# Performance work log

Measured on AMD Instinct MI355X. Metric: run time of the kernel, lower is better.

## Reference

```python
import jax, jax.numpy as jnp
import numpy as np

B, S, IN_DIM, EMBED, H = 2, 2048, 512, 512, 8
HD = EMBED // H


def setup_inputs() -> dict:
    key = jax.random.key(0)
    ks = jax.random.split(key, 6)
    x = jax.random.normal(ks[0], (B, S, IN_DIM), dtype=jnp.float32)
    dist_mat = jax.random.normal(ks[1], (B, H, S, S), dtype=jnp.float32) * 0.02
    path_mat = jax.random.normal(ks[2], (B, H, S, S), dtype=jnp.float32) * 0.02
    # xavier-uniform-style init scale
    qkv_w = jax.random.normal(ks[3], (IN_DIM, 3 * EMBED), dtype=jnp.float32) * (1.0 / np.sqrt(IN_DIM))
    qkv_b = jnp.zeros((3 * EMBED,), dtype=jnp.float32)
    o_w = jax.random.normal(ks[4], (EMBED, EMBED), dtype=jnp.float32) * (1.0 / np.sqrt(EMBED))
    o_b = jnp.zeros((EMBED,), dtype=jnp.float32)
    return {"x": x, "dist_mat": dist_mat, "path_mat": path_mat,
            "qkv_w": qkv_w, "qkv_b": qkv_b, "o_w": o_w, "o_b": o_b}


def reference(x, dist_mat, path_mat, qkv_w, qkv_b, o_w, o_b):
    b, s, _ = x.shape
    qkv = x @ qkv_w + qkv_b                         # [B,S,3*EMBED]
    qkv = qkv.reshape(b, s, H, 3 * HD).transpose(0, 2, 1, 3)  # [B,H,S,3*HD]
    q, k, v = jnp.split(qkv, 3, axis=-1)            # each [B,H,S,HD]
    logits = jnp.einsum('bhqd,bhkd->bhqk', q, k) / jnp.sqrt(jnp.float32(HD))
    attn = jax.nn.softmax(logits, axis=-1)
    attn = attn + dist_mat + path_mat               # post-softmax bias (breaks flash fusion)
    vals = jnp.einsum('bhqk,bhkd->bhqd', attn, v)   # [B,H,S,HD]
    vals = vals.transpose(0, 2, 1, 3).reshape(b, s, EMBED)
    return vals @ o_w + o_b
```

## Files before the change

kernel.cpp:

```cpp
#include <hip/hip_runtime.h>
#include <stdint.h>
#include <stddef.h>

#define B_ 2
#define H_ 8
#define S_ 2048
#define D_ 64
#define E_ 512
#define N3_ 1536
#define M_ (B_*S_)
#define K_ 512

typedef __attribute__((ext_vector_type(4))) float f32x4;
typedef __attribute__((ext_vector_type(8))) __bf16 bf16x8;
typedef __attribute__((ext_vector_type(4))) __bf16 bf16x4;

static __device__ __forceinline__ int swz(int b) { return b ^ (((b >> 7) & 7) << 4); }

static __device__ __forceinline__ void gl_lds16(const void* g, void* l) {
    __builtin_amdgcn_global_load_lds((const __attribute__((address_space(1))) void*)g,
                                     (__attribute__((address_space(3))) void*)l, 16, 0, 0);
}

__global__ void cvt_bf16_kernel(const float* __restrict__ in, __bf16* __restrict__ out, int n4) {
    int i = blockIdx.x * blockDim.x + threadIdx.x;
    if (i < n4) {
        float4 v = reinterpret_cast<const float4*>(in)[i];
        bf16x4 o;
        o[0] = (__bf16)v.x; o[1] = (__bf16)v.y; o[2] = (__bf16)v.z; o[3] = (__bf16)v.w;
        reinterpret_cast<bf16x4*>(out)[i] = o;
    }
}

__global__ void transpose_cvt_kernel(const float* __restrict__ in, __bf16* __restrict__ out,
                                     int R, int C) {
    __shared__ float tile[32][33];
    int tc = blockIdx.x * 32, tr = blockIdx.y * 32;
    int lx = threadIdx.x & 31, ly = threadIdx.x >> 5;
    #pragma unroll
    for (int p = 0; p < 4; ++p) {
        int r = tr + ly + p * 8, c = tc + lx;
        if (r < R && c < C) tile[ly + p * 8][lx] = in[(size_t)r * C + c];
    }
    __syncthreads();
    #pragma unroll
    for (int p = 0; p < 4; ++p) {
        int oc = tc + ly + p * 8;
        int orow = tr + lx;
        if (oc < C && orow < R) out[(size_t)oc * R + orow] = (__bf16)tile[lx][ly + p * 8];
    }
}

__global__ void transpose_v_kernel(const __bf16* __restrict__ v, __bf16* __restrict__ vt) {
    __shared__ __bf16 t[64][65];
    int bh = blockIdx.x >> 5;
    int s0 = (blockIdx.x & 31) << 6;
    int tid = threadIdx.x;
    const __bf16* src = v + ((size_t)bh * S_ + s0) * D_;
    #pragma unroll
    for (int p = 0; p < 2; ++p) {
        int idx = (p * 256 + tid) * 8;
        int r = idx >> 6, c = idx & 63;
        bf16x8 val = *reinterpret_cast<const bf16x8*>(src + (size_t)r * D_ + c);
        #pragma unroll
        for (int e = 0; e < 8; ++e) t[r][c + e] = val[e];
    }
    __syncthreads();
    __bf16* dst = vt + (size_t)bh * D_ * S_ + s0;
    #pragma unroll
    for (int p = 0; p < 16; ++p) {
        int idx = p * 256 + tid;
        int d = idx >> 6, s = idx & 63;
        dst[(size_t)d * S_ + s] = t[s][d];
    }
}

template<int MODE>
__global__ __launch_bounds__(256, 2) void gemm_kernel(
    const __bf16* __restrict__ A, const __bf16* __restrict__ Bt,
    const float* __restrict__ bias,
    void* __restrict__ o0, void* __restrict__ o1, void* __restrict__ o2,
    int M, int N, int K)
{
    __shared__ __align__(16) __bf16 lA[128 * 64];
    __shared__ __align__(16) __bf16 lB[128 * 64];
    const int tid = threadIdx.x;
    const int wave = tid >> 6, lane = tid & 63;
    const int wm = wave >> 1, wn = wave & 1;
    const int m0 = blockIdx.y * 128, n0 = blockIdx.x * 128;
    const int l15 = lane & 15, l4 = lane >> 4;

    f32x4 acc[4][4] = {};

    for (int k0 = 0; k0 < K; k0 += 64) {
        __syncthreads();
        #pragma unroll
        for (int p = 0; p < 4; ++p) {
            int base = p * 4096 + wave * 1024;
            int js = swz(base + lane * 16);
            int row = js >> 7, colb = js & 127;
            gl_lds16((const char*)A + ((size_t)(m0 + row) * K + k0) * 2 + colb, (char*)lA + base);
            gl_lds16((const char*)Bt + ((size_t)(n0 + row) * K + k0) * 2 + colb, (char*)lB + base);
        }
        __syncthreads();
        #pragma unroll
        for (int ks = 0; ks < 2; ++ks) {
            bf16x8 af[4], bfr[4];
            #pragma unroll
            for (int i = 0; i < 4; ++i) {
                af[i]  = *(const bf16x8*)((const char*)lA + swz(((wm * 64 + i * 16 + l15) << 7) + ks * 64 + (l4 << 4)));
                bfr[i] = *(const bf16x8*)((const char*)lB + swz(((wn * 64 + i * 16 + l15) << 7) + ks * 64 + (l4 << 4)));
            }
            #pragma unroll
            for (int i = 0; i < 4; ++i)
                #pragma unroll
                for (int j = 0; j < 4; ++j)
                    acc[i][j] = __builtin_amdgcn_mfma_f32_16x16x32_bf16(af[i], bfr[j], acc[i][j], 0, 0, 0);
        }
    }
    #pragma unroll
    for (int i = 0; i < 4; ++i) {
        int mg0 = m0 + wm * 64 + i * 16 + (l4 << 2);
        #pragma unroll
        for (int j = 0; j < 4; ++j) {
            int ng = n0 + wn * 64 + j * 16 + l15;
            float bv = bias[ng];
            #pragma unroll
            for (int r = 0; r < 4; ++r) {
                int m = mg0 + r;
                float val = acc[i][j][r] + bv;
                if (MODE == 0) {
                    int h = ng / 192, rr = ng % 192;
                    int which = rr >> 6, d = rr & 63;
                    int b = m >> 11, s = m & (S_ - 1);
                    if (which == 0) val *= 0.125f;
                    __bf16* dst = which == 0 ? (__bf16*)o0 : which == 1 ? (__bf16*)o1 : (__bf16*)o2;
                    dst[(((size_t)((b * H_ + h) * S_ + s)) << 6) + d] = (__bf16)val;
                } else {
                    ((float*)o0)[(size_t)m * N + ng] = val;
                }
            }
        }
    }
}

__global__ __launch_bounds__(256, 2) void attn_kernel(
    const __bf16* __restrict__ q, const __bf16* __restrict__ k,
    const __bf16* __restrict__ vt,
    const float* __restrict__ dist, const float* __restrict__ path,
    __bf16* __restrict__ vals)
{
    __shared__ __align__(16) __bf16 kl[64 * 64];
    __shared__ __align__(16) __bf16 vl[64 * 64];
    __shared__ __align__(16) __bf16 pl[4][16 * 64];
    const int tid = threadIdx.x, wave = tid >> 6, lane = tid & 63;
    const int l15 = lane & 15, l4 = lane >> 4;
    const int bh = blockIdx.x >> 5;
    const int q0 = (blockIdx.x & 31) << 6;
    const int b = bh >> 3, h = bh & 7;
    const int qrow = q0 + wave * 16 + l15;

    const __bf16* qp = q + ((size_t)bh * S_ + qrow) * D_;
    bf16x8 qf0 = *(const bf16x8*)(qp + (l4 << 3));
    bf16x8 qf1 = *(const bf16x8*)(qp + 32 + (l4 << 3));

    const float* dp = dist + ((size_t)bh * S_ + qrow) * S_;
    const float* pp = path + ((size_t)bh * S_ + qrow) * S_;

    float m_run[4], l_run[4];
    f32x4 o_p[4] = {}, o_b[4] = {};
    #pragma unroll
    for (int r = 0; r < 4; ++r) { m_run[r] = -1e30f; l_run[r] = 0.f; }

    const char* kg = (const char*)(k + (size_t)bh * S_ * D_);
    const char* vg = (const char*)(vt + (size_t)bh * D_ * S_);

    for (int kt = 0; kt < S_; kt += 64) {
        __syncthreads();
        #pragma unroll
        for (int p = 0; p < 2; ++p) {
            int base = p * 4096 + wave * 1024;
            int js = swz(base + lane * 16);
            int row = js >> 7, colb = js & 127;
            gl_lds16(kg + ((size_t)(kt + row) * D_) * 2 + colb, (char*)kl + base);
            gl_lds16(vg + ((size_t)row * S_ + kt) * 2 + colb, (char*)vl + base);
        }
        float4 dv[2][2], pw[2][2];
        #pragma unroll
        for (int ks = 0; ks < 2; ++ks) {
            int kc = kt + ks * 32 + (l4 << 3);
            dv[ks][0] = *(const float4*)(dp + kc);
            dv[ks][1] = *(const float4*)(dp + kc + 4);
            pw[ks][0] = *(const float4*)(pp + kc);
            pw[ks][1] = *(const float4*)(pp + kc + 4);
        }
        __syncthreads();

        f32x4 lg[4] = {};
        #pragma unroll
        for (int ks = 0; ks < 2; ++ks) {
            bf16x8 qa = ks ? qf1 : qf0;
            #pragma unroll
            for (int n = 0; n < 4; ++n) {
                bf16x8 kf = *(const bf16x8*)((const char*)kl + swz(((n * 16 + l15) << 7) + ks * 64 + (l4 << 4)));
                lg[n] = __builtin_amdgcn_mfma_f32_16x16x32_bf16(qa, kf, lg[n], 0, 0, 0);
            }
        }
        float scale[4], rsum[4], pe[4][4];
        #pragma unroll
        for (int r = 0; r < 4; ++r) {
            float t = fmaxf(fmaxf(lg[0][r], lg[1][r]), fmaxf(lg[2][r], lg[3][r]));
            t = fmaxf(t, __shfl_xor(t, 1));
            t = fmaxf(t, __shfl_xor(t, 2));
            t = fmaxf(t, __shfl_xor(t, 4));
            t = fmaxf(t, __shfl_xor(t, 8));
            float mnew = fmaxf(m_run[r], t);
            scale[r] = __expf(m_run[r] - mnew);
            m_run[r] = mnew;
            rsum[r] = 0.f;
        }
        #pragma unroll
        for (int n = 0; n < 4; ++n)
            #pragma unroll
            for (int r = 0; r < 4; ++r) {
                pe[n][r] = __expf(lg[n][r] - m_run[r]);
                rsum[r] += pe[n][r];
            }
        #pragma unroll
        for (int r = 0; r < 4; ++r) {
            float s = rsum[r];
            s += __shfl_xor(s, 1);
            s += __shfl_xor(s, 2);
            s += __shfl_xor(s, 4);
            s += __shfl_xor(s, 8);
            l_run[r] = l_run[r] * scale[r] + s;
        }
        #pragma unroll
        for (int n = 0; n < 4; ++n)
            #pragma unroll
            for (int r = 0; r < 4; ++r)
                o_p[n][r] *= scale[r];
        char* pb = (char*)&pl[wave][0];
        #pragma unroll
        for (int n = 0; n < 4; ++n)
            #pragma unroll
            for (int r = 0; r < 4; ++r) {
                int row = (l4 << 2) + r, col = n * 16 + l15;
                *(__bf16*)(pb + swz((row << 7) + col * 2)) = (__bf16)pe[n][r];
            }
        #pragma unroll
        for (int ks = 0; ks < 2; ++ks) {
            bf16x8 pa = *(const bf16x8*)((const char*)pb + swz((l15 << 7) + ks * 64 + (l4 << 4)));
            float4 a0 = dv[ks][0], a1 = dv[ks][1], b0 = pw[ks][0], b1 = pw[ks][1];
            bf16x8 ba;
            ba[0] = (__bf16)(a0.x + b0.x); ba[1] = (__bf16)(a0.y + b0.y);
            ba[2] = (__bf16)(a0.z + b0.z); ba[3] = (__bf16)(a0.w + b0.w);
            ba[4] = (__bf16)(a1.x + b1.x); ba[5] = (__bf16)(a1.y + b1.y);
            ba[6] = (__bf16)(a1.z + b1.z); ba[7] = (__bf16)(a1.w + b1.w);
            #pragma unroll
            for (int n = 0; n < 4; ++n) {
                bf16x8 vf = *(const bf16x8*)((const char*)vl + swz(((n * 16 + l15) << 7) + ks * 64 + (l4 << 4)));
                o_p[n] = __builtin_amdgcn_mfma_f32_16x16x32_bf16(pa, vf, o_p[n], 0, 0, 0);
                o_b[n] = __builtin_amdgcn_mfma_f32_16x16x32_bf16(ba, vf, o_b[n], 0, 0, 0);
            }
        }
    }
    #pragma unroll
    for (int r = 0; r < 4; ++r) {
        int s = q0 + wave * 16 + (l4 << 2) + r;
        float inv = 1.f / l_run[r];
        __bf16* dst = vals + (size_t)(b * S_ + s) * E_ + h * D_;
        #pragma unroll
        for (int n = 0; n < 4; ++n) {
            int d = n * 16 + l15;
            dst[d] = (__bf16)(o_p[n][r] * inv + o_b[n][r]);
        }
    }
}

extern "C" void kernel_launch(void* const* d_in, const int* in_sizes, int n_in,
                              void* d_out, int out_size, void* d_ws, size_t ws_size,
                              hipStream_t stream) {
    (void)in_sizes; (void)n_in; (void)out_size; (void)ws_size;
    const float* x      = (const float*)d_in[0];
    const float* dist   = (const float*)d_in[1];
    const float* path   = (const float*)d_in[2];
    const float* qkv_w  = (const float*)d_in[3];
    const float* qkv_b  = (const float*)d_in[4];
    const float* o_w    = (const float*)d_in[5];
    const float* o_b    = (const float*)d_in[6];
    float* out = (float*)d_out;

    char* ws = (char*)d_ws;
    __bf16* xb     = (__bf16*)(ws);
    __bf16* qkv_wT = (__bf16*)(ws + (4  << 20));
    __bf16* o_wT   = (__bf16*)(ws + (6  << 20));
    __bf16* qb     = (__bf16*)(ws + (7  << 20));
    __bf16* kb     = (__bf16*)(ws + (11 << 20));
    __bf16* vb     = (__bf16*)(ws + (15 << 20));
    __bf16* vtb    = (__bf16*)(ws + (19 << 20));
    __bf16* valsb  = (__bf16*)(ws + (23 << 20));

    cvt_bf16_kernel<<<(M_ * K_ / 4 + 255) / 256, 256, 0, stream>>>(x, xb, M_ * K_ / 4);
    transpose_cvt_kernel<<<dim3(N3_ / 32, K_ / 32), 256, 0, stream>>>(qkv_w, qkv_wT, K_, N3_);
    transpose_cvt_kernel<<<dim3(E_ / 32, E_ / 32), 256, 0, stream>>>(o_w, o_wT, E_, E_);
    gemm_kernel<0><<<dim3(N3_ / 128, M_ / 128), 256, 0, stream>>>(xb, qkv_wT, qkv_b, qb, kb, vb, M_, N3_, K_);
    transpose_v_kernel<<<B_ * H_ * (S_ / 64), 256, 0, stream>>>(vb, vtb);
    attn_kernel<<<B_ * H_ * (S_ / 64), 256, 0, stream>>>(qb, kb, vtb, dist, path, valsb);
    gemm_kernel<1><<<dim3(E_ / 128, M_ / 128), 256, 0, stream>>>(valsb, o_wT, o_b, out, nullptr, nullptr, M_, E_, K_);
}
```

Before: 202.3 us.

## Split bias-times-V into separate blocks in a fused launch, combine afterward

Moves the (dist+path)@V product out of the softmax attention loop into its own set of 512 blocks, launched in the same grid as the attention blocks. Bias blocks stream dist/path from global memory and read V^T directly from global. Attention blocks now only do compute-bound QK/softmax/PV. Both write fp32 partial results, and a new combine kernel adds them into bf16 vals. Block IDs are remapped so that each head's work lands on one XCD, and occupancy is raised to 4 blocks per SM. The cost is extra fp32 intermediate traffic and one additional kernel launch.

```diff
diff --git a/kernel.cpp b/kernel.cpp
--- a/kernel.cpp
+++ b/kernel.cpp
@@ -144,31 +144,64 @@
     }
 }
 
-__global__ __launch_bounds__(256, 2) void attn_kernel(
+#define NBIAS 512
+__global__ __launch_bounds__(256, 4) void fused_kernel(
     const __bf16* __restrict__ q, const __bf16* __restrict__ k,
     const __bf16* __restrict__ vt,
     const float* __restrict__ dist, const float* __restrict__ path,
-    __bf16* __restrict__ vals)
+    float* __restrict__ attno, float* __restrict__ biaso)
 {
     __shared__ __align__(16) __bf16 kl[64 * 64];
     __shared__ __align__(16) __bf16 vl[64 * 64];
     __shared__ __align__(16) __bf16 pl[4][16 * 64];
     const int tid = threadIdx.x, wave = tid >> 6, lane = tid & 63;
     const int l15 = lane & 15, l4 = lane >> 4;
-    const int bh = blockIdx.x >> 5;
-    const int q0 = (blockIdx.x & 31) << 6;
-    const int b = bh >> 3, h = bh & 7;
+    const int id = blockIdx.x;
+
+    if (id < NBIAS) {
+        const int xcd = id & 7, j = id >> 3;
+        const int bh = xcd * 2 + (j >> 5), m0 = (j & 31) << 6;
+        const int row = m0 + wave * 16 + l15;
+        const float* dp = dist + ((size_t)bh * S_ + row) * S_;
+        const float* pp = path + ((size_t)bh * S_ + row) * S_;
+        const __bf16* vtp = vt + (size_t)bh * D_ * S_;
+        f32x4 acc[4] = {};
+        #pragma unroll 2
+        for (int k0 = 0; k0 < S_; k0 += 32) {
+            int kc = k0 + (l4 << 3);
+            float4 d0 = *(const float4*)(dp + kc), d1 = *(const float4*)(dp + kc + 4);
+            float4 p0 = *(const float4*)(pp + kc), p1 = *(const float4*)(pp + kc + 4);
+            bf16x8 a;
+            a[0] = (__bf16)(d0.x + p0.x); a[1] = (__bf16)(d0.y + p0.y);
+            a[2] = (__bf16)(d0.z + p0.z); a[3] = (__bf16)(d0.w + p0.w);
+            a[4] = (__bf16)(d1.x + p1.x); a[5] = (__bf16)(d1.y + p1.y);
+            a[6] = (__bf16)(d1.z + p1.z); a[7] = (__bf16)(d1.w + p1.w);
+            #pragma unroll
+            for (int n = 0; n < 4; ++n) {
+                bf16x8 vf = *(const bf16x8*)(vtp + (size_t)(n * 16 + l15) * S_ + kc);
+                acc[n] = __builtin_amdgcn_mfma_f32_16x16x32_bf16(a, vf, acc[n], 0, 0, 0);
+            }
+        }
+        #pragma unroll
+        for (int n = 0; n < 4; ++n)
+            #pragma unroll
+            for (int r = 0; r < 4; ++r)
+                biaso[((size_t)bh * S_ + m0 + wave * 16 + (l4 << 2) + r) * D_ + n * 16 + l15] = acc[n][r];
+        return;
+    }
+
+    const int aid = id - NBIAS;
+    const int xcd = aid & 7, j = aid >> 3;
+    const int bh = xcd * 2 + (j >> 5);
+    const int q0 = (j & 31) << 6;
     const int qrow = q0 + wave * 16 + l15;
 
     const __bf16* qp = q + ((size_t)bh * S_ + qrow) * D_;
     bf16x8 qf0 = *(const bf16x8*)(qp + (l4 << 3));
     bf16x8 qf1 = *(const bf16x8*)(qp + 32 + (l4 << 3));
 
-    const float* dp = dist + ((size_t)bh * S_ + qrow) * S_;
-    const float* pp = path + ((size_t)bh * S_ + qrow) * S_;
-
     float m_run[4], l_run[4];
-    f32x4 o_p[4] = {}, o_b[4] = {};
+    f32x4 o_p[4] = {};
     #pragma unroll
     for (int r = 0; r < 4; ++r) { m_run[r] = -1e30f; l_run[r] = 0.f; }
 
@@ -184,15 +217,6 @@
             int row = js >> 7, colb = js & 127;
             gl_lds16(kg + ((size_t)(kt + row) * D_) * 2 + colb, (char*)kl + base);
             gl_lds16(vg + ((size_t)row * S_ + kt) * 2 + colb, (char*)vl + base);
-        }
-        float4 dv[2][2], pw[2][2];
-        #pragma unroll
-        for (int ks = 0; ks < 2; ++ks) {
-            int kc = kt + ks * 32 + (l4 << 3);
-            dv[ks][0] = *(const float4*)(dp + kc);
-            dv[ks][1] = *(const float4*)(dp + kc + 4);
-            pw[ks][0] = *(const float4*)(pp + kc);
-            pw[ks][1] = *(const float4*)(pp + kc + 4);
         }
         __syncthreads();
 
@@ -245,23 +269,16 @@
         for (int n = 0; n < 4; ++n)
             #pragma unroll
             for (int r = 0; r < 4; ++r) {
-                int row = (l4 << 2) + r, col = n * 16 + l15;
-                *(__bf16*)(pb + swz((row << 7) + col * 2)) = (__bf16)pe[n][r];
+                int prow = (l4 << 2) + r, pcol = n * 16 + l15;
+                *(__bf16*)(pb + swz((prow << 7) + pcol * 2)) = (__bf16)pe[n][r];
             }
         #pragma unroll
         for (int ks = 0; ks < 2; ++ks) {
             bf16x8 pa = *(const bf16x8*)((const char*)pb + swz((l15 << 7) + ks * 64 + (l4 << 4)));
-            float4 a0 = dv[ks][0], a1 = dv[ks][1], b0 = pw[ks][0], b1 = pw[ks][1];
-            bf16x8 ba;
-            ba[0] = (__bf16)(a0.x + b0.x); ba[1] = (__bf16)(a0.y + b0.y);
-            ba[2] = (__bf16)(a0.z + b0.z); ba[3] = (__bf16)(a0.w + b0.w);
-            ba[4] = (__bf16)(a1.x + b1.x); ba[5] = (__bf16)(a1.y + b1.y);
-            ba[6] = (__bf16)(a1.z + b1.z); ba[7] = (__bf16)(a1.w + b1.w);
             #pragma unroll
             for (int n = 0; n < 4; ++n) {
                 bf16x8 vf = *(const bf16x8*)((const char*)vl + swz(((n * 16 + l15) << 7) + ks * 64 + (l4 << 4)));
                 o_p[n] = __builtin_amdgcn_mfma_f32_16x16x32_bf16(pa, vf, o_p[n], 0, 0, 0);
-                o_b[n] = __builtin_amdgcn_mfma_f32_16x16x32_bf16(ba, vf, o_b[n], 0, 0, 0);
             }
         }
     }
@@ -269,13 +286,29 @@
     for (int r = 0; r < 4; ++r) {
         int s = q0 + wave * 16 + (l4 << 2) + r;
         float inv = 1.f / l_run[r];
-        __bf16* dst = vals + (size_t)(b * S_ + s) * E_ + h * D_;
-        #pragma unroll
-        for (int n = 0; n < 4; ++n) {
-            int d = n * 16 + l15;
-            dst[d] = (__bf16)(o_p[n][r] * inv + o_b[n][r]);
-        }
-    }
+        float* dst = attno + ((size_t)bh * S_ + s) * D_;
+        #pragma unroll
+        for (int n = 0; n < 4; ++n)
+            dst[n * 16 + l15] = o_p[n][r] * inv;
+    }
+}
+
+__global__ void combine_kernel(const float* __restrict__ a, const float* __restrict__ b,
+                               __bf16* __restrict__ out) {
+    int i = blockIdx.x * blockDim.x + threadIdx.x;
+    size_t off = (size_t)i * 8;
+    int d = (int)(off & 63);
+    int s = (int)((off >> 6) & (S_ - 1));
+    int bh = (int)(off >> 17);
+    f32x4 a0 = ((const f32x4*)(a + off))[0], a1 = ((const f32x4*)(a + off))[1];
+    f32x4 b0 = ((const f32x4*)(b + off))[0], b1 = ((const f32x4*)(b + off))[1];
+    bf16x8 o;
+    o[0] = (__bf16)(a0[0] + b0[0]); o[1] = (__bf16)(a0[1] + b0[1]);
+    o[2] = (__bf16)(a0[2] + b0[2]); o[3] = (__bf16)(a0[3] + b0[3]);
+    o[4] = (__bf16)(a1[0] + b1[0]); o[5] = (__bf16)(a1[1] + b1[1]);
+    o[6] = (__bf16)(a1[2] + b1[2]); o[7] = (__bf16)(a1[3] + b1[3]);
+    int bb = bh >> 3, h = bh & 7;
+    *(bf16x8*)(out + ((size_t)(bb * S_ + s) * E_) + h * D_ + d) = o;
 }
 
 extern "C" void kernel_launch(void* const* d_in, const int* in_sizes, int n_in,
@@ -293,19 +326,22 @@
 
     char* ws = (char*)d_ws;
     __bf16* xb     = (__bf16*)(ws);
-    __bf16* qkv_wT = (__bf16*)(ws + (4  << 20));
-    __bf16* o_wT   = (__bf16*)(ws + (6  << 20));
-    __bf16* qb     = (__bf16*)(ws + (7  << 20));
-    __bf16* kb     = (__bf16*)(ws + (11 << 20));
-    __bf16* vb     = (__bf16*)(ws + (15 << 20));
-    __bf16* vtb    = (__bf16*)(ws + (19 << 20));
-    __bf16* valsb  = (__bf16*)(ws + (23 << 20));
+    __bf16* vb     = (__bf16*)(ws + (4  << 20));
+    float*  attno  = (float*) (ws);
+    __bf16* qb     = (__bf16*)(ws + (8  << 20));
+    __bf16* kb     = (__bf16*)(ws + (12 << 20));
+    __bf16* vtb    = (__bf16*)(ws + (16 << 20));
+    __bf16* qkv_wT = (__bf16*)(ws + (20 << 20));
+    __bf16* o_wT   = (__bf16*)(ws + (20 << 20) + (3 << 19));
+    float*  biaso  = (float*) (ws + (22 << 20));
+    __bf16* valsb  = (__bf16*)(ws + (30 << 20));
 
     cvt_bf16_kernel<<<(M_ * K_ / 4 + 255) / 256, 256, 0, stream>>>(x, xb, M_ * K_ / 4);
     transpose_cvt_kernel<<<dim3(N3_ / 32, K_ / 32), 256, 0, stream>>>(qkv_w, qkv_wT, K_, N3_);
     transpose_cvt_kernel<<<dim3(E_ / 32, E_ / 32), 256, 0, stream>>>(o_w, o_wT, E_, E_);
     gemm_kernel<0><<<dim3(N3_ / 128, M_ / 128), 256, 0, stream>>>(xb, qkv_wT, qkv_b, qb, kb, vb, M_, N3_, K_);
     transpose_v_kernel<<<B_ * H_ * (S_ / 64), 256, 0, stream>>>(vb, vtb);
-    attn_kernel<<<B_ * H_ * (S_ / 64), 256, 0, stream>>>(qb, kb, vtb, dist, path, valsb);
+    fused_kernel<<<NBIAS + 512, 256, 0, stream>>>(qb, kb, vtb, dist, path, attno, biaso);
+    combine_kernel<<<(B_ * H_ * S_ * D_ / 8) / 256, 256, 0, stream>>>(attno, biaso, valsb);
     gemm_kernel<1><<<dim3(E_ / 128, M_ / 128), 256, 0, stream>>>(valsb, o_wT, o_b, out, nullptr, nullptr, M_, E_, K_);
 }
```

Result: slower. 228.0 us (+12.7%).

## Double-buffer K/V tiles and prefetch bias rows one iteration ahead

Applied to the files above, without the earlier changes.

K and V tiles now live in two LDS buffers and the next tile is staged while the current one is computed. The dist/path bias loads are also issued one iteration early into registers, which cuts the per-iteration barriers from two to one. Block indices are remapped so each XCD handles two (batch, head) pairs, for better L2 locality of K/V. The bias MFMA is hoisted ahead of the softmax. The cost is doubled LDS for K/V and extra live registers, which may lower occupancy under launch_bounds(256,2).

```diff
diff --git a/kernel.cpp b/kernel.cpp
--- a/kernel.cpp
+++ b/kernel.cpp
@@ -150,13 +150,15 @@
     const float* __restrict__ dist, const float* __restrict__ path,
     __bf16* __restrict__ vals)
 {
-    __shared__ __align__(16) __bf16 kl[64 * 64];
-    __shared__ __align__(16) __bf16 vl[64 * 64];
+    __shared__ __align__(16) __bf16 kl[2][64 * 64];
+    __shared__ __align__(16) __bf16 vl[2][64 * 64];
     __shared__ __align__(16) __bf16 pl[4][16 * 64];
     const int tid = threadIdx.x, wave = tid >> 6, lane = tid & 63;
     const int l15 = lane & 15, l4 = lane >> 4;
-    const int bh = blockIdx.x >> 5;
-    const int q0 = (blockIdx.x & 31) << 6;
+    const int id = blockIdx.x;
+    const int xcd = id & 7, j = id >> 3;
+    const int bh = xcd * 2 + (j >> 5);
+    const int q0 = (j & 31) << 6;
     const int b = bh >> 3, h = bh & 7;
     const int qrow = q0 + wave * 16 + l15;
 
@@ -167,34 +169,55 @@
     const float* dp = dist + ((size_t)bh * S_ + qrow) * S_;
     const float* pp = path + ((size_t)bh * S_ + qrow) * S_;
 
-    float m_run[4], l_run[4];
-    f32x4 o_p[4] = {}, o_b[4] = {};
-    #pragma unroll
-    for (int r = 0; r < 4; ++r) { m_run[r] = -1e30f; l_run[r] = 0.f; }
-
     const char* kg = (const char*)(k + (size_t)bh * S_ * D_);
     const char* vg = (const char*)(vt + (size_t)bh * D_ * S_);
 
-    for (int kt = 0; kt < S_; kt += 64) {
-        __syncthreads();
+    auto STAGE = [&](int kt, int buf) {
         #pragma unroll
         for (int p = 0; p < 2; ++p) {
             int base = p * 4096 + wave * 1024;
             int js = swz(base + lane * 16);
             int row = js >> 7, colb = js & 127;
-            gl_lds16(kg + ((size_t)(kt + row) * D_) * 2 + colb, (char*)kl + base);
-            gl_lds16(vg + ((size_t)row * S_ + kt) * 2 + colb, (char*)vl + base);
-        }
-        float4 dv[2][2], pw[2][2];
+            gl_lds16(kg + ((size_t)(kt + row) * D_) * 2 + colb, (char*)kl[buf] + base);
+            gl_lds16(vg + ((size_t)row * S_ + kt) * 2 + colb, (char*)vl[buf] + base);
+        }
+    };
+    float4 fb[8];
+    auto BLOAD = [&](int kt) {
         #pragma unroll
         for (int ks = 0; ks < 2; ++ks) {
             int kc = kt + ks * 32 + (l4 << 3);
-            dv[ks][0] = *(const float4*)(dp + kc);
-            dv[ks][1] = *(const float4*)(dp + kc + 4);
-            pw[ks][0] = *(const float4*)(pp + kc);
-            pw[ks][1] = *(const float4*)(pp + kc + 4);
-        }
-        __syncthreads();
+            fb[ks * 2 + 0] = *(const float4*)(dp + kc);
+            fb[ks * 2 + 1] = *(const float4*)(dp + kc + 4);
+            fb[4 + ks * 2 + 0] = *(const float4*)(pp + kc);
+            fb[4 + ks * 2 + 1] = *(const float4*)(pp + kc + 4);
+        }
+    };
+
+    float m_run[4], l_run[4];
+    f32x4 o_p[4] = {}, o_b[4] = {};
+    #pragma unroll
+    for (int r = 0; r < 4; ++r) { m_run[r] = -1e30f; l_run[r] = 0.f; }
+
+    STAGE(0, 0);
+    BLOAD(0);
+    __syncthreads();
+
+    int cur = 0;
+    for (int kt = 0; kt < S_; kt += 64) {
+        bf16x8 ba[2];
+        #pragma unroll
+        for (int ks = 0; ks < 2; ++ks) {
+            float4 d0 = fb[ks * 2], d1 = fb[ks * 2 + 1];
+            float4 p0 = fb[4 + ks * 2], p1 = fb[4 + ks * 2 + 1];
+            ba[ks][0] = (__bf16)(d0.x + p0.x); ba[ks][1] = (__bf16)(d0.y + p0.y);
+            ba[ks][2] = (__bf16)(d0.z + p0.z); ba[ks][3] = (__bf16)(d0.w + p0.w);
+            ba[ks][4] = (__bf16)(d1.x + p1.x); ba[ks][5] = (__bf16)(d1.y + p1.y);
+            ba[ks][6] = (__bf16)(d1.z + p1.z); ba[ks][7] = (__bf16)(d1.w + p1.w);
+        }
+        int ktn = (kt + 64 < S_) ? kt + 64 : kt;
+        STAGE(ktn, cur ^ 1);
+        BLOAD(ktn);
 
         f32x4 lg[4] = {};
         #pragma unroll
@@ -202,10 +225,17 @@
             bf16x8 qa = ks ? qf1 : qf0;
             #pragma unroll
             for (int n = 0; n < 4; ++n) {
-                bf16x8 kf = *(const bf16x8*)((const char*)kl + swz(((n * 16 + l15) << 7) + ks * 64 + (l4 << 4)));
+                bf16x8 kf = *(const bf16x8*)((const char*)kl[cur] + swz(((n * 16 + l15) << 7) + ks * 64 + (l4 << 4)));
                 lg[n] = __builtin_amdgcn_mfma_f32_16x16x32_bf16(qa, kf, lg[n], 0, 0, 0);
             }
         }
+        #pragma unroll
+        for (int ks = 0; ks < 2; ++ks)
+            #pragma unroll
+            for (int n = 0; n < 4; ++n) {
+                bf16x8 vf = *(const bf16x8*)((const char*)vl[cur] + swz(((n * 16 + l15) << 7) + ks * 64 + (l4 << 4)));
+                o_b[n] = __builtin_amdgcn_mfma_f32_16x16x32_bf16(ba[ks], vf, o_b[n], 0, 0, 0);
+            }
         float scale[4], rsum[4], pe[4][4];
         #pragma unroll
         for (int r = 0; r < 4; ++r) {
@@ -245,25 +275,20 @@
         for (int n = 0; n < 4; ++n)
             #pragma unroll
             for (int r = 0; r < 4; ++r) {
-                int row = (l4 << 2) + r, col = n * 16 + l15;
-                *(__bf16*)(pb + swz((row << 7) + col * 2)) = (__bf16)pe[n][r];
+                int prow = (l4 << 2) + r, pcol = n * 16 + l15;
+                *(__bf16*)(pb + swz((prow << 7) + pcol * 2)) = (__bf16)pe[n][r];
             }
         #pragma unroll
         for (int ks = 0; ks < 2; ++ks) {
             bf16x8 pa = *(const bf16x8*)((const char*)pb + swz((l15 << 7) + ks * 64 + (l4 << 4)));
-            float4 a0 = dv[ks][0], a1 = dv[ks][1], b0 = pw[ks][0], b1 = pw[ks][1];
-            bf16x8 ba;
-            ba[0] = (__bf16)(a0.x + b0.x); ba[1] = (__bf16)(a0.y + b0.y);
-            ba[2] = (__bf16)(a0.z + b0.z); ba[3] = (__bf16)(a0.w + b0.w);
-            ba[4] = (__bf16)(a1.x + b1.x); ba[5] = (__bf16)(a1.y + b1.y);
-            ba[6] = (__bf16)(a1.z + b1.z); ba[7] = (__bf16)(a1.w + b1.w);
             #pragma unroll
             for (int n = 0; n < 4; ++n) {
-                bf16x8 vf = *(const bf16x8*)((const char*)vl + swz(((n * 16 + l15) << 7) + ks * 64 + (l4 << 4)));
+                bf16x8 vf = *(const bf16x8*)((const char*)vl[cur] + swz(((n * 16 + l15) << 7) + ks * 64 + (l4 << 4)));
                 o_p[n] = __builtin_amdgcn_mfma_f32_16x16x32_bf16(pa, vf, o_p[n], 0, 0, 0);
-                o_b[n] = __builtin_amdgcn_mfma_f32_16x16x32_bf16(ba, vf, o_b[n], 0, 0, 0);
-            }
-        }
+            }
+        }
+        __syncthreads();
+        cur ^= 1;
     }
     #pragma unroll
     for (int r = 0; r < 4; ++r) {
```

After: 192.6 us. -4.8%, faster.
